# Kernel tuning notes

Measured on AMD Instinct MI355X. Metric: run time of the kernel, lower is better.

The kernel has to match this reference:

```python
import jax, jax.numpy as jnp
import numpy as np

B, D, H, W, C = 2, 8, 128, 128, 64
HEADS, DH = 4, 16
EPS = 1e-12  # torch F.normalize eps


def setup_inputs() -> dict:
    key = jax.random.key(0)
    ks = jax.random.split(key, 8)
    rn = lambda k, shp, s: jax.random.normal(k, shp, jnp.float32) * s
    return {
        "x_in": rn(ks[0], (B, D, H, W, C), 1.0),
        "Wq": rn(ks[1], (C, HEADS * DH), 0.05),
        "Wk": rn(ks[2], (C, HEADS * DH), 0.05),
        "Wv": rn(ks[3], (C, HEADS * DH), 0.05),
        "rescale": jnp.ones((HEADS, 1, 1), jnp.float32),
        "Wproj": rn(ks[4], (HEADS * DH, C), 0.05),
        "bproj": jnp.zeros((C,), jnp.float32),
        "Wpos1": rn(ks[5], (C, 1, 3, 3, 3), 0.1),
        "Wpos2": rn(ks[6], (C, 1, 3, 3, 3), 0.1),
    }


def _l2norm(x):
    # torch F.normalize(p=2, dim=-1): x / max(||x||, eps)
    return x / jnp.maximum(jnp.linalg.norm(x, axis=-1, keepdims=True), EPS)


def _dwconv3d(x, w):
    # depthwise Conv3d, kernel 3, stride 1, padding 1, groups = channels
    return jax.lax.conv_general_dilated(
        x, w, (1, 1, 1), 'SAME',
        dimension_numbers=('NCDHW', 'OIDHW', 'NCDHW'),
        feature_group_count=w.shape[0])


def reference(x_in, Wq, Wk, Wv, rescale, Wproj, bproj, Wpos1, Wpos2):
    b, d, h, w, c = x_in.shape
    n = d * h * w
    x = x_in.reshape(b, n, c)
    v_inp = x @ Wv                                   # [b, n, heads*dh]
    # [b, heads, dh, n] layout (attention over channel dim)
    q = jnp.transpose((x @ Wq).reshape(b, n, HEADS, DH), (0, 2, 3, 1))
    k = jnp.transpose((x @ Wk).reshape(b, n, HEADS, DH), (0, 2, 3, 1))
    v = jnp.transpose(v_inp.reshape(b, n, HEADS, DH), (0, 2, 3, 1))
    q = _l2norm(q)
    k = _l2norm(k)
    attn = jnp.einsum('bhdn,bhen->bhde', k, q) * rescale  # [b, heads, dh, dh]
    attn = jax.nn.softmax(attn, axis=-1)
    out = jnp.einsum('bhde,bhen->bhdn', attn, v)          # [b, heads, dh, n]
    out = jnp.transpose(out, (0, 3, 1, 2)).reshape(b, n, HEADS * DH)
    out_c = (out @ Wproj + bproj).reshape(b, d, h, w, c)
    # positional branch: depthwise conv -> GELU -> depthwise conv on v_inp
    vv = jnp.transpose(v_inp.reshape(b, d, h, w, c), (0, 4, 1, 2, 3))  # NCDHW
    p = _dwconv3d(vv, Wpos1)
    p = jax.nn.gelu(p, approximate=False)
    p = _dwconv3d(p, Wpos2)
    out_p = jnp.transpose(p, (0, 2, 3, 4, 1))
    return out_c + out_p
```

## Files before the change

### kernel.cpp

```cpp
#include <hip/hip_runtime.h>
#include <math.h>

#define DD 8
#define HH 128
#define WW2 128
#define NPT 131072
#define NTOT 262144
#define NBK 8

typedef __attribute__((ext_vector_type(8))) short short8;
typedef __attribute__((ext_vector_type(4))) float f32x4;
typedef __attribute__((ext_vector_type(4))) unsigned short u16x4;
typedef __attribute__((ext_vector_type(8))) unsigned short u16x8;
typedef unsigned short u16;

static const size_t OFF_P1  = 0;
static const size_t OFF_P2  = 33554432;
static const size_t OFF_V   = 67108864;
static const size_t OFF_PW  = 100663296;
static const size_t OFF_PM  = 100687872;
static const size_t OFF_FLAG= 100704256;
static const size_t OFF_CW  = 100704768;
static const size_t OFF_PART= 134217728;
#define SP_F    0
#define WQ_F    65536
#define WK_F    69632
#define WV_F    73728
#define CW_WPROJ 0
#define CW_WPOS1 4096
#define CW_WPOS2 5824
#define CW_RESC  7552
#define CW_BPROJ 7556
#define CW_ATT   7680

__device__ __forceinline__ float bf2f(u16 u){
  unsigned int x = ((unsigned int)u) << 16;
  return __builtin_bit_cast(float, x);
}
__device__ __forceinline__ u16 f2bf(float f){
  unsigned int x = __builtin_bit_cast(unsigned int, f);
  unsigned int r = (x + 0x7fffu + ((x >> 16) & 1u)) >> 16;
  return (u16)r;
}

__device__ __forceinline__ float fgelu(float o){
  float z  = o * 0.70710678118654752f;
  float az = fabsf(z);
  float t1 = __builtin_amdgcn_rcpf(fmaf(0.3275911f, az, 1.f));
  float poly = t1 * fmaf(t1, fmaf(t1, fmaf(t1, fmaf(t1, 1.061405429f,
               -1.453152027f), 1.421413741f), -0.284496736f), 0.254829592f);
  float ex = __expf(-z * z);
  float er = 1.f - poly * ex;
  er = (z < 0.f) ? -er : er;
  return 0.5f * o * (1.f + er);
}

__device__ __forceinline__ int probe_isf32(const void* x, int t){
  u16 u = ((const u16*)x)[2 * (t & 63)];
  int e = (u >> 7) & 0xFF;
  int plaus = (u == 0) || (u == 0x8000u) || (e >= 100 && e <= 130);
  unsigned long long m = __ballot(plaus);
  return (__popcll(m) < 48) ? 1 : 0;
}

__global__ __launch_bounds__(256) void k_prep(const void* __restrict__ x,
    const void* __restrict__ Wproj, const void* __restrict__ rescale,
    const void* __restrict__ bproj, const void* __restrict__ Wpos1,
    const void* __restrict__ Wpos2, const void* __restrict__ Wq,
    const void* __restrict__ Wk, const void* __restrict__ Wv,
    int* __restrict__ flag, float* __restrict__ cw, float* __restrict__ gpart,
    u16* __restrict__ packW){
  __shared__ int sflag;
  int t = threadIdx.x, blk = blockIdx.x;
  if (t < 64){
    int f = probe_isf32(x, t);
    if (t == 0) sflag = f;
  }
  __syncthreads();
  int isf32 = sflag;
  if (blk < 32){
    for (int i = blk * 2048 + t; i < (blk + 1) * 2048; i += 256)
      gpart[i] = 0.f;
    if (blk == 0){
      if (t == 0) *flag = isf32;
      auto conv = [&](const void* src, float* dst, int n){
        for (int i = t; i < n; i += 256)
          dst[i] = isf32 ? ((const float*)src)[i] : bf2f(((const u16*)src)[i]);
      };
      conv(Wproj, cw + CW_WPROJ, 4096);
      conv(Wpos1, cw + CW_WPOS1, 1728);
      conv(Wpos2, cw + CW_WPOS2, 1728);
      conv(rescale, cw + CW_RESC, 4);
      conv(bproj,   cw + CW_BPROJ, 64);
      conv(Wq, gpart + WQ_F, 4096);
      conv(Wk, gpart + WK_F, 4096);
      conv(Wv, gpart + WV_F, 4096);
    }
  } else {
    int o = (blk - 32) * 256 + t;
    int f = o >> 9, l = (o >> 3) & 63, j = o & 7;
    int tt = f >> 1, s = f & 1;
    int k = s * 32 + (l >> 4) * 8 + j;
    int n = tt * 16 + (l & 15);
    int idx = k * 64 + n;
    float val = isf32 ? ((const float*)Wv)[idx] : bf2f(((const u16*)Wv)[idx]);
    packW[o] = f2bf(val);
  }
}

__device__ __forceinline__ short8 ld8_adapt(const void* p, size_t idx, int isf32){
  if (!isf32) return *(const short8*)((const u16*)p + idx);
  const float4* f = (const float4*)((const float*)p + idx);
  float4 u = f[0], v2 = f[1];
  short8 r;
  r[0] = (short)f2bf(u.x);  r[1] = (short)f2bf(u.y);
  r[2] = (short)f2bf(u.z);  r[3] = (short)f2bf(u.w);
  r[4] = (short)f2bf(v2.x); r[5] = (short)f2bf(v2.y);
  r[6] = (short)f2bf(v2.z); r[7] = (short)f2bf(v2.w);
  return r;
}

__device__ __forceinline__ short8 pack8(float4 u, float4 v2){
  short8 r;
  r[0] = (short)f2bf(u.x);  r[1] = (short)f2bf(u.y);
  r[2] = (short)f2bf(u.z);  r[3] = (short)f2bf(u.w);
  r[4] = (short)f2bf(v2.x); r[5] = (short)f2bf(v2.y);
  r[6] = (short)f2bf(v2.z); r[7] = (short)f2bf(v2.w);
  return r;
}

__global__ __launch_bounds__(512) void k_qkv(const void* __restrict__ x,
                                             const int* __restrict__ flag,
                                             const u16* __restrict__ packW,
                                             u16* __restrict__ vT,
                                             float* __restrict__ Sp){
  __shared__ u16 sXT[64][136];
  int isf32 = *flag;
  int wave = threadIdx.x >> 6, lane = threadIdx.x & 63;
  int m = lane & 15, quad = lane >> 4;
  const short8* bw = (const short8*)packW;
  short8 bv[8];
#pragma unroll
  for (int f = 0; f < 8; f++) bv[f] = bw[f * 64 + lane];
  int c1 = wave >> 1, c2p = (wave & 1) * 2;
  f32x4 aS[2];
  aS[0] = (f32x4)(0.f); aS[1] = (f32x4)(0.f);

  int pbase = blockIdx.x * 512;
  int b = pbase >> 17;

  size_t rb0 = (size_t)(pbase + wave * 16 + m) * 64;
  short8 a0 = ld8_adapt(x, rb0 + quad * 8, isf32);
  short8 a1 = ld8_adapt(x, rb0 + 32 + quad * 8, isf32);

  for (int s = 0; s < 4; s++){
    int p0 = pbase + s * 128 + wave * 16;
    f32x4 av[4];
#pragma unroll
    for (int t = 0; t < 4; t++) av[t] = (f32x4)(0.f);
#pragma unroll
    for (int t = 0; t < 4; t++){
      av[t] = __builtin_amdgcn_mfma_f32_16x16x32_bf16(a0, bv[t * 2 + 0], av[t], 0, 0, 0);
      av[t] = __builtin_amdgcn_mfma_f32_16x16x32_bf16(a1, bv[t * 2 + 1], av[t], 0, 0, 0);
    }
    int nloc = p0 & (NPT - 1);
#pragma unroll
    for (int t = 0; t < 4; t++){
      u16x4 pk;
#pragma unroll
      for (int r = 0; r < 4; r++) pk[r] = f2bf(av[t][r]);
      *(u16x4*)(vT + ((size_t)(b * 64 + t * 16 + m)) * NPT + nloc + quad * 4) = pk;
    }
    float4 pf0a, pf0b, pf1a, pf1b; short8 ps0, ps1;
    if (s < 3){
      size_t rbn = (size_t)(pbase + (s + 1) * 128 + wave * 16 + m) * 64;
      if (isf32){
        const float4* f0 = (const float4*)((const float*)x + rbn + quad * 8);
        pf0a = f0[0]; pf0b = f0[1];
        const float4* f1 = (const float4*)((const float*)x + rbn + 32 + quad * 8);
        pf1a = f1[0]; pf1b = f1[1];
      } else {
        ps0 = *(const short8*)((const u16*)x + rbn + quad * 8);
        ps1 = *(const short8*)((const u16*)x + rbn + 32 + quad * 8);
      }
    }
    if (s) __syncthreads();
#pragma unroll
    for (int j = 0; j < 8; j++){
      sXT[quad * 8 + j][wave * 16 + m]      = (u16)a0[j];
      sXT[32 + quad * 8 + j][wave * 16 + m] = (u16)a1[j];
    }
    __syncthreads();
#pragma unroll
    for (int ks = 0; ks < 4; ks++){
      short8 fA  = *(const short8*)&sXT[c1 * 16 + m][ks * 32 + quad * 8];
      short8 fB0 = *(const short8*)&sXT[(c2p + 0) * 16 + m][ks * 32 + quad * 8];
      short8 fB1 = *(const short8*)&sXT[(c2p + 1) * 16 + m][ks * 32 + quad * 8];
      aS[0] = __builtin_amdgcn_mfma_f32_16x16x32_bf16(fA, fB0, aS[0], 0, 0, 0);
      aS[1] = __builtin_amdgcn_mfma_f32_16x16x32_bf16(fA, fB1, aS[1], 0, 0, 0);
    }
    if (s < 3){
      if (isf32){ a0 = pack8(pf0a, pf0b); a1 = pack8(pf1a, pf1b); }
      else      { a0 = ps0;               a1 = ps1; }
    }
  }
  int bk = blockIdx.x & (NBK - 1);
  float* Sb = Sp + (size_t)(bk * 2 + b) * 4096;
#pragma unroll
  for (int tt = 0; tt < 2; tt++)
#pragma unroll
    for (int r = 0; r < 4; r++)
      atomicAdd(&Sb[(c1 * 16 + quad * 4 + r) * 64 + (c2p + tt) * 16 + m], aS[tt][r]);
}

__global__ __launch_bounds__(256) void k_attn_h(const float* __restrict__ Sp,
    const float* __restrict__ wqk, const float* __restrict__ cw,
    float* __restrict__ Aout){
  __shared__ float sS[64 * 65];
  __shared__ float sWh[1024];
  __shared__ float sT[1024];
  __shared__ float sG[256];
  __shared__ float sNq[16], sNk[16];
  int blk = blockIdx.x, t = threadIdx.x;
  int b = blk >> 2, h = blk & 3;
  for (int i = t; i < 4096; i += 256){
    float s = 0.f;
#pragma unroll
    for (int bk = 0; bk < NBK; bk++) s += Sp[(size_t)(bk * 2 + b) * 4096 + i];
    sS[(i >> 6) * 65 + (i & 63)] = s;
  }
  for (int i = t; i < 1024; i += 256)
    sWh[i] = wqk[(i >> 4) * 64 + h * 16 + (i & 15)];
  __syncthreads();
  int cc = t & 63, eg = t >> 6;
  {
    float a0 = 0.f, a1 = 0.f, a2 = 0.f, a3 = 0.f;
    for (int c2 = 0; c2 < 64; c2++){
      float sv = sS[cc * 65 + c2];
      a0 = fmaf(sv, sWh[c2 * 16 + eg * 4 + 0], a0);
      a1 = fmaf(sv, sWh[c2 * 16 + eg * 4 + 1], a1);
      a2 = fmaf(sv, sWh[c2 * 16 + eg * 4 + 2], a2);
      a3 = fmaf(sv, sWh[c2 * 16 + eg * 4 + 3], a3);
    }
    sT[cc * 16 + eg * 4 + 0] = a0;
    sT[cc * 16 + eg * 4 + 1] = a1;
    sT[cc * 16 + eg * 4 + 2] = a2;
    sT[cc * 16 + eg * 4 + 3] = a3;
  }
  __syncthreads();
  if (t < 16){
    float a = 0.f;
    for (int c = 0; c < 64; c++) a += sWh[c * 16 + t] * sT[c * 16 + t];
    sNq[t] = a;
  }
  __syncthreads();
  for (int i = t; i < 1024; i += 256)
    sWh[i] = wqk[4096 + (i >> 4) * 64 + h * 16 + (i & 15)];
  __syncthreads();
  {
    int d = t >> 4, e = t & 15;
    float a = 0.f;
    for (int c = 0; c < 64; c++) a += sWh[c * 16 + d] * sT[c * 16 + e];
    sG[d * 16 + e] = a;
  }
  __syncthreads();
  {
    float a0 = 0.f, a1 = 0.f, a2 = 0.f, a3 = 0.f;
    for (int c2 = 0; c2 < 64; c2++){
      float sv = sS[cc * 65 + c2];
      a0 = fmaf(sv, sWh[c2 * 16 + eg * 4 + 0], a0);
      a1 = fmaf(sv, sWh[c2 * 16 + eg * 4 + 1], a1);
      a2 = fmaf(sv, sWh[c2 * 16 + eg * 4 + 2], a2);
      a3 = fmaf(sv, sWh[c2 * 16 + eg * 4 + 3], a3);
    }
    __syncthreads();
    sT[cc * 16 + eg * 4 + 0] = a0;
    sT[cc * 16 + eg * 4 + 1] = a1;
    sT[cc * 16 + eg * 4 + 2] = a2;
    sT[cc * 16 + eg * 4 + 3] = a3;
  }
  __syncthreads();
  if (t < 16){
    float a = 0.f;
    for (int c = 0; c < 64; c++) a += sWh[c * 16 + t] * sT[c * 16 + t];
    sNk[t] = a;
  }
  __syncthreads();
  if (t < 16){
    int d = t;
    float nk = fmaxf(sqrtf(sNk[d]), 1e-12f);
    float rs = cw[CW_RESC + h];
    float lg[16]; float mx = -1e30f;
#pragma unroll
    for (int e = 0; e < 16; e++){
      float nq = fmaxf(sqrtf(sNq[e]), 1e-12f);
      float L = sG[d * 16 + e] / (nk * nq) * rs;
      lg[e] = L; mx = fmaxf(mx, L);
    }
    float sum = 0.f;
#pragma unroll
    for (int e = 0; e < 16; e++){ lg[e] = expf(lg[e] - mx); sum += lg[e]; }
    float inv = 1.f / sum;
#pragma unroll
    for (int e = 0; e < 16; e++)
      Aout[((b * 4 + h) << 8) + d * 16 + e] = lg[e] * inv;
  }
}

__global__ __launch_bounds__(256) void k_fold(const float* __restrict__ Aout,
    const float* __restrict__ cw, const float* __restrict__ Wvf,
    u16* __restrict__ packM){
  __shared__ float sM[4096];
  int b = blockIdx.x, t = threadIdx.x;
  for (int i = t; i < 4096; i += 256){
    int he = i >> 6, c = i & 63;
    int h = he >> 4, e = he & 15;
    float acc = 0.f;
#pragma unroll
    for (int d = 0; d < 16; d++)
      acc += Aout[b * 1024 + h * 256 + d * 16 + e] * cw[CW_WPROJ + (h * 16 + d) * 64 + c];
    sM[i] = acc;
  }
  __syncthreads();
  for (int i = t; i < 4096; i += 256){
    int f = i >> 9, l = (i >> 3) & 63, j = i & 7;
    int t4 = f >> 1, s2 = f & 1;
    int k = s2 * 32 + (l >> 4) * 8 + j;
    int n = t4 * 16 + (l & 15);
    float acc = 0.f;
#pragma unroll 8
    for (int he = 0; he < 64; he++)
      acc += Wvf[k * 64 + he] * sM[he * 64 + n];
    packM[b * 4096 + i] = f2bf(acc);
  }
}

template <bool GELU>
__global__ __launch_bounds__(256, 3) void k_dwconv(const u16* __restrict__ src,
    const float* __restrict__ wpos, u16* __restrict__ dst){
  int xi = threadIdx.x & 15, ty = threadIdx.x >> 4;
  int zp = ty >> 2, yq = ty & 3;
  int x0 = xi * 8;
  int c  = blockIdx.x;
  int y0 = blockIdx.y * 8 + yq * 2;
  int b  = blockIdx.z;
  int z0 = zp * 2;
  const float* wg = wpos + c * 27;
  float w27[27];
#pragma unroll
  for (int i = 0; i < 27; i++) w27[i] = wg[i];
  const u16* plane = src + (size_t)(b * 64 + c) * NPT;

  short8 raw[16];
  float  msk[16];
#pragma unroll
  for (int iz = 0; iz < 4; iz++){
    int zz = z0 - 1 + iz;
    int zc = zz < 0 ? 0 : (zz > DD - 1 ? DD - 1 : zz);
    float zm = (zz == zc) ? 1.f : 0.f;
#pragma unroll
    for (int iy = 0; iy < 4; iy++){
      int yy = y0 - 1 + iy;
      int yc = yy < 0 ? 0 : (yy > HH - 1 ? HH - 1 : yy);
      raw[iz * 4 + iy] = *(const short8*)(plane + zc * 16384 + yc * 128 + x0);
      msk[iz * 4 + iy] = zm * ((yy == yc) ? 1.f : 0.f);
    }
  }

  float acc[2][2][8];
#pragma unroll
  for (int dz = 0; dz < 2; dz++)
#pragma unroll
    for (int dy = 0; dy < 2; dy++)
#pragma unroll
      for (int xx = 0; xx < 8; xx++) acc[dz][dy][xx] = 0.f;

#pragma unroll
  for (int iz = 0; iz < 4; iz++){
#pragma unroll
    for (int iy = 0; iy < 4; iy++){
      short8 mid = raw[iz * 4 + iy];
      float m = msk[iz * 4 + iy];
      float row[10];
#pragma unroll
      for (int e = 0; e < 8; e++) row[1 + e] = bf2f((u16)mid[e]);
      float lf = __shfl_up(row[8], 1);
      float rg = __shfl_down(row[1], 1);
      row[0] = (xi > 0)  ? lf : 0.f;
      row[9] = (xi < 15) ? rg : 0.f;
#pragma unroll
      for (int e = 0; e < 10; e++) row[e] *= m;
#pragma unroll
      for (int dzi = 0; dzi < 2; dzi++){
        int kd = iz - dzi;
        if (kd < 0 || kd > 2) continue;
#pragma unroll
        for (int dyi = 0; dyi < 2; dyi++){
          int kh = iy - dyi;
          if (kh < 0 || kh > 2) continue;
#pragma unroll
          for (int kw = 0; kw < 3; kw++){
            float w = w27[kd * 9 + kh * 3 + kw];
#pragma unroll
            for (int xx = 0; xx < 8; xx++)
              acc[dzi][dyi][xx] = fmaf(row[xx + kw], w, acc[dzi][dyi][xx]);
          }
        }
      }
    }
  }
#pragma unroll
  for (int dzi = 0; dzi < 2; dzi++){
    int zo = z0 + dzi;
#pragma unroll
    for (int dyi = 0; dyi < 2; dyi++){
      int yo = y0 + dyi;
      u16x8 pk;
#pragma unroll
      for (int xx = 0; xx < 8; xx++){
        float o = acc[dzi][dyi][xx];
        if (GELU) o = fgelu(o);
        pk[xx] = f2bf(o);
      }
      *(u16x8*)(dst + (size_t)(b * 64 + c) * NPT + zo * 16384 + yo * 128 + x0) = pk;
    }
  }
}

__global__ __launch_bounds__(256) void k_final(const void* __restrict__ x,
                                               const int* __restrict__ flag,
                                               const u16* __restrict__ packM,
                                               const float* __restrict__ bprojf,
                                               const u16* __restrict__ p2T,
                                               float* __restrict__ out){
  int isf32 = *flag;
  int wave = threadIdx.x >> 6, lane = threadIdx.x & 63;
  int m = lane & 15, quad = lane >> 4;
  int p0 = blockIdx.x * 64 + wave * 16;
  int b = p0 >> 17;
  int nloc = p0 & (NPT - 1);
  size_t rowbase = (size_t)(p0 + m) * 64;
  short8 a0 = ld8_adapt(x, rowbase + quad * 8, isf32);
  short8 a1 = ld8_adapt(x, rowbase + 32 + quad * 8, isf32);
  const short8* bm = (const short8*)(packM + (size_t)b * 4096);
  f32x4 acc[4];
#pragma unroll
  for (int t = 0; t < 4; t++) acc[t] = (f32x4)(0.f);
#pragma unroll
  for (int t = 0; t < 4; t++){
    short8 b0 = bm[(t * 2 + 0) * 64 + lane];
    short8 b1 = bm[(t * 2 + 1) * 64 + lane];
    acc[t] = __builtin_amdgcn_mfma_f32_16x16x32_bf16(a0, b0, acc[t], 0, 0, 0);
    acc[t] = __builtin_amdgcn_mfma_f32_16x16x32_bf16(a1, b1, acc[t], 0, 0, 0);
  }
#pragma unroll
  for (int t = 0; t < 4; t++){
    int c = t * 16 + m;
    float bias = bprojf[c];
    u16x4 pv = *(const u16x4*)(p2T + (size_t)(b * 64 + c) * NPT + nloc + quad * 4);
#pragma unroll
    for (int r = 0; r < 4; r++){
      size_t p = (size_t)p0 + quad * 4 + r;
      out[p * 64 + c] = acc[t][r] + bias + bf2f(pv[r]);
    }
  }
}

extern "C" void kernel_launch(void* const* d_in, const int* in_sizes, int n_in,
                              void* d_out, int out_size, void* d_ws, size_t ws_size,
                              hipStream_t stream){
  (void)in_sizes; (void)n_in; (void)out_size; (void)ws_size;
  const void* x      = d_in[0];
  const void* Wq     = d_in[1];
  const void* Wk     = d_in[2];
  const void* Wv     = d_in[3];
  const void* rescale= d_in[4];
  const void* Wproj  = d_in[5];
  const void* bproj  = d_in[6];
  const void* Wpos1  = d_in[7];
  const void* Wpos2  = d_in[8];

  char* ws = (char*)d_ws;
  u16* p1T   = (u16*)(ws + OFF_P1);
  u16* p2T   = (u16*)(ws + OFF_P2);
  u16* vT    = (u16*)(ws + OFF_V);
  u16* packW = (u16*)(ws + OFF_PW);
  u16* packM = (u16*)(ws + OFF_PM);
  int* flag  = (int*)(ws + OFF_FLAG);
  float* cw  = (float*)(ws + OFF_CW);
  float* part= (float*)(ws + OFF_PART);
  float* Sp  = part + SP_F;
  float* wqk = part + WQ_F;
  float* Wvf = part + WV_F;
  float* Aout= cw + CW_ATT;
  float* out = (float*)d_out;

  k_prep<<<48, 256, 0, stream>>>(x, Wproj, rescale, bproj, Wpos1, Wpos2, Wq, Wk, Wv,
                                 flag, cw, Sp, packW);
  k_qkv<<<NTOT / 512, 512, 0, stream>>>(x, flag, packW, vT, Sp);
  k_attn_h<<<8, 256, 0, stream>>>(Sp, wqk, cw, Aout);
  k_fold<<<2, 256, 0, stream>>>(Aout, cw, Wvf, packM);
  k_dwconv<true><<<dim3(64, 16, 2), 256, 0, stream>>>(vT, cw + CW_WPOS1, p1T);
  k_dwconv<false><<<dim3(64, 16, 2), 256, 0, stream>>>(p1T, cw + CW_WPOS2, p2T);
  k_final<<<NTOT / 64, 256, 0, stream>>>(x, flag, packM, cw + CW_BPROJ, p2T, out);
}
```

Before: 298.5 us.

## Fold attention-projection into attn kernel and feed final GEMM from stored V

k_qkv now also writes V in row-major bf16 (vP), so k_final multiplies V by the per-batch attention·Wproj matrix instead of x by a Wv-folded matrix. This removes the k_fold kernel and its 64-deep Wv fold: k_attn_h computes the 16x64 attn·Wproj block per head and writes packM directly. In exchange it adds an extra 32 MB scattered 2-byte store stream from k_qkv, and the x prefetch across stages in k_qkv is dropped. It also adds a second bf16 rounding (V stored as bf16 before the final GEMM).

```diff
diff --git a/kernel.cpp b/kernel.cpp
--- a/kernel.cpp
+++ b/kernel.cpp
@@ -22,16 +22,15 @@
 static const size_t OFF_FLAG= 100704256;
 static const size_t OFF_CW  = 100704768;
 static const size_t OFF_PART= 134217728;
+static const size_t OFF_VP  = 150994944;
 #define SP_F    0
 #define WQ_F    65536
 #define WK_F    69632
-#define WV_F    73728
 #define CW_WPROJ 0
 #define CW_WPOS1 4096
 #define CW_WPOS2 5824
 #define CW_RESC  7552
 #define CW_BPROJ 7556
-#define CW_ATT   7680
 
 __device__ __forceinline__ float bf2f(u16 u){
   unsigned int x = ((unsigned int)u) << 16;
@@ -94,7 +93,6 @@
       conv(bproj,   cw + CW_BPROJ, 64);
       conv(Wq, gpart + WQ_F, 4096);
       conv(Wk, gpart + WK_F, 4096);
-      conv(Wv, gpart + WV_F, 4096);
     }
   } else {
     int o = (blk - 32) * 256 + t;
@@ -120,19 +118,11 @@
   return r;
 }
 
-__device__ __forceinline__ short8 pack8(float4 u, float4 v2){
-  short8 r;
-  r[0] = (short)f2bf(u.x);  r[1] = (short)f2bf(u.y);
-  r[2] = (short)f2bf(u.z);  r[3] = (short)f2bf(u.w);
-  r[4] = (short)f2bf(v2.x); r[5] = (short)f2bf(v2.y);
-  r[6] = (short)f2bf(v2.z); r[7] = (short)f2bf(v2.w);
-  return r;
-}
-
 __global__ __launch_bounds__(512) void k_qkv(const void* __restrict__ x,
                                              const int* __restrict__ flag,
                                              const u16* __restrict__ packW,
                                              u16* __restrict__ vT,
+                                             u16* __restrict__ vP,
                                              float* __restrict__ Sp){
   __shared__ u16 sXT[64][136];
   int isf32 = *flag;
@@ -149,12 +139,11 @@
   int pbase = blockIdx.x * 512;
   int b = pbase >> 17;
 
-  size_t rb0 = (size_t)(pbase + wave * 16 + m) * 64;
-  short8 a0 = ld8_adapt(x, rb0 + quad * 8, isf32);
-  short8 a1 = ld8_adapt(x, rb0 + 32 + quad * 8, isf32);
-
   for (int s = 0; s < 4; s++){
     int p0 = pbase + s * 128 + wave * 16;
+    size_t rowbase = (size_t)(p0 + m) * 64;
+    short8 a0 = ld8_adapt(x, rowbase + quad * 8, isf32);
+    short8 a1 = ld8_adapt(x, rowbase + 32 + quad * 8, isf32);
     f32x4 av[4];
 #pragma unroll
     for (int t = 0; t < 4; t++) av[t] = (f32x4)(0.f);
@@ -170,19 +159,9 @@
 #pragma unroll
       for (int r = 0; r < 4; r++) pk[r] = f2bf(av[t][r]);
       *(u16x4*)(vT + ((size_t)(b * 64 + t * 16 + m)) * NPT + nloc + quad * 4) = pk;
-    }
-    float4 pf0a, pf0b, pf1a, pf1b; short8 ps0, ps1;
-    if (s < 3){
-      size_t rbn = (size_t)(pbase + (s + 1) * 128 + wave * 16 + m) * 64;
-      if (isf32){
-        const float4* f0 = (const float4*)((const float*)x + rbn + quad * 8);
-        pf0a = f0[0]; pf0b = f0[1];
-        const float4* f1 = (const float4*)((const float*)x + rbn + 32 + quad * 8);
-        pf1a = f1[0]; pf1b = f1[1];
-      } else {
-        ps0 = *(const short8*)((const u16*)x + rbn + quad * 8);
-        ps1 = *(const short8*)((const u16*)x + rbn + 32 + quad * 8);
-      }
+#pragma unroll
+      for (int r = 0; r < 4; r++)
+        vP[(size_t)(p0 + quad * 4 + r) * 64 + t * 16 + m] = pk[r];
     }
     if (s) __syncthreads();
 #pragma unroll
@@ -199,10 +178,6 @@
       aS[0] = __builtin_amdgcn_mfma_f32_16x16x32_bf16(fA, fB0, aS[0], 0, 0, 0);
       aS[1] = __builtin_amdgcn_mfma_f32_16x16x32_bf16(fA, fB1, aS[1], 0, 0, 0);
     }
-    if (s < 3){
-      if (isf32){ a0 = pack8(pf0a, pf0b); a1 = pack8(pf1a, pf1b); }
-      else      { a0 = ps0;               a1 = ps1; }
-    }
   }
   int bk = blockIdx.x & (NBK - 1);
   float* Sb = Sp + (size_t)(bk * 2 + b) * 4096;
@@ -215,11 +190,12 @@
 
 __global__ __launch_bounds__(256) void k_attn_h(const float* __restrict__ Sp,
     const float* __restrict__ wqk, const float* __restrict__ cw,
-    float* __restrict__ Aout){
+    u16* __restrict__ packM){
   __shared__ float sS[64 * 65];
   __shared__ float sWh[1024];
   __shared__ float sT[1024];
   __shared__ float sG[256];
+  __shared__ float sA[256];
   __shared__ float sNq[16], sNk[16];
   int blk = blockIdx.x, t = threadIdx.x;
   int b = blk >> 2, h = blk & 3;
@@ -286,6 +262,8 @@
     sNk[t] = a;
   }
   __syncthreads();
+  for (int i = t; i < 1024; i += 256)
+    sT[i] = cw[CW_WPROJ + (h * 16 + (i >> 6)) * 64 + (i & 63)];
   if (t < 16){
     int d = t;
     float nk = fmaxf(sqrtf(sNk[d]), 1e-12f);
@@ -302,36 +280,20 @@
     for (int e = 0; e < 16; e++){ lg[e] = expf(lg[e] - mx); sum += lg[e]; }
     float inv = 1.f / sum;
 #pragma unroll
-    for (int e = 0; e < 16; e++)
-      Aout[((b * 4 + h) << 8) + d * 16 + e] = lg[e] * inv;
-  }
-}
-
-__global__ __launch_bounds__(256) void k_fold(const float* __restrict__ Aout,
-    const float* __restrict__ cw, const float* __restrict__ Wvf,
-    u16* __restrict__ packM){
-  __shared__ float sM[4096];
-  int b = blockIdx.x, t = threadIdx.x;
-  for (int i = t; i < 4096; i += 256){
-    int he = i >> 6, c = i & 63;
-    int h = he >> 4, e = he & 15;
+    for (int e = 0; e < 16; e++) sA[d * 16 + e] = lg[e] * inv;
+  }
+  __syncthreads();
+#pragma unroll
+  for (int q = 0; q < 4; q++){
+    int i = q * 256 + t;
+    int t4 = i >> 8, lhi = (i >> 7) & 1, llo = (i >> 3) & 15, j = i & 7;
+    int e = lhi * 8 + j, c = t4 * 16 + llo;
     float acc = 0.f;
 #pragma unroll
-    for (int d = 0; d < 16; d++)
-      acc += Aout[b * 1024 + h * 256 + d * 16 + e] * cw[CW_WPROJ + (h * 16 + d) * 64 + c];
-    sM[i] = acc;
-  }
-  __syncthreads();
-  for (int i = t; i < 4096; i += 256){
-    int f = i >> 9, l = (i >> 3) & 63, j = i & 7;
-    int t4 = f >> 1, s2 = f & 1;
-    int k = s2 * 32 + (l >> 4) * 8 + j;
-    int n = t4 * 16 + (l & 15);
-    float acc = 0.f;
-#pragma unroll 8
-    for (int he = 0; he < 64; he++)
-      acc += Wvf[k * 64 + he] * sM[he * 64 + n];
-    packM[b * 4096 + i] = f2bf(acc);
+    for (int d = 0; d < 16; d++) acc += sA[d * 16 + e] * sT[d * 64 + c];
+    int f = t4 * 2 + (h >> 1);
+    int l = (2 * (h & 1) + lhi) * 16 + llo;
+    packM[b * 4096 + f * 512 + l * 8 + j] = f2bf(acc);
   }
 }
 
@@ -427,21 +389,19 @@
   }
 }
 
-__global__ __launch_bounds__(256) void k_final(const void* __restrict__ x,
-                                               const int* __restrict__ flag,
+__global__ __launch_bounds__(256) void k_final(const u16* __restrict__ vP,
                                                const u16* __restrict__ packM,
                                                const float* __restrict__ bprojf,
                                                const u16* __restrict__ p2T,
                                                float* __restrict__ out){
-  int isf32 = *flag;
   int wave = threadIdx.x >> 6, lane = threadIdx.x & 63;
   int m = lane & 15, quad = lane >> 4;
   int p0 = blockIdx.x * 64 + wave * 16;
   int b = p0 >> 17;
   int nloc = p0 & (NPT - 1);
   size_t rowbase = (size_t)(p0 + m) * 64;
-  short8 a0 = ld8_adapt(x, rowbase + quad * 8, isf32);
-  short8 a1 = ld8_adapt(x, rowbase + 32 + quad * 8, isf32);
+  short8 a0 = *(const short8*)(vP + rowbase + quad * 8);
+  short8 a1 = *(const short8*)(vP + rowbase + 32 + quad * 8);
   const short8* bm = (const short8*)(packM + (size_t)b * 4096);
   f32x4 acc[4];
 #pragma unroll
@@ -484,6 +444,7 @@
   u16* p1T   = (u16*)(ws + OFF_P1);
   u16* p2T   = (u16*)(ws + OFF_P2);
   u16* vT    = (u16*)(ws + OFF_V);
+  u16* vP    = (u16*)(ws + OFF_VP);
   u16* packW = (u16*)(ws + OFF_PW);
   u16* packM = (u16*)(ws + OFF_PM);
   int* flag  = (int*)(ws + OFF_FLAG);
@@ -491,16 +452,13 @@
   float* part= (float*)(ws + OFF_PART);
   float* Sp  = part + SP_F;
   float* wqk = part + WQ_F;
-  float* Wvf = part + WV_F;
-  float* Aout= cw + CW_ATT;
   float* out = (float*)d_out;
 
   k_prep<<<48, 256, 0, stream>>>(x, Wproj, rescale, bproj, Wpos1, Wpos2, Wq, Wk, Wv,
                                  flag, cw, Sp, packW);
-  k_qkv<<<NTOT / 512, 512, 0, stream>>>(x, flag, packW, vT, Sp);
-  k_attn_h<<<8, 256, 0, stream>>>(Sp, wqk, cw, Aout);
-  k_fold<<<2, 256, 0, stream>>>(Aout, cw, Wvf, packM);
+  k_qkv<<<NTOT / 512, 512, 0, stream>>>(x, flag, packW, vT, vP, Sp);
+  k_attn_h<<<8, 256, 0, stream>>>(Sp, wqk, cw, packM);
   k_dwconv<true><<<dim3(64, 16, 2), 256, 0, stream>>>(vT, cw + CW_WPOS1, p1T);
   k_dwconv<false><<<dim3(64, 16, 2), 256, 0, stream>>>(p1T, cw + CW_WPOS2, p2T);
-  k_final<<<NTOT / 64, 256, 0, stream>>>(x, flag, packM, cw + CW_BPROJ, p2T, out);
-}
+  k_final<<<NTOT / 64, 256, 0, stream>>>(vP, packM, cw + CW_BPROJ, p2T, out);
+}
```

New measurement: 264.4 us. 11.4% less time.
